# Kernel tuning notes

Hardware: AMD Instinct MI355X
Metric: run time of the kernel (lower is better)

The kernel has to match this reference:

```python
import jax, jax.numpy as jnp
import numpy as np


def _token2map(tok, loc, h, w):
    # scatter-add tokens onto an h x w grid. forward uses kernel_size=1, so the
    # Gaussian inpainting branch (reconstruct_feature) is a no-op and omitted.
    B, Nt, C = tok.shape
    loc = jnp.clip(loc, -1.0, 1.0)
    px = 0.5 * (loc + 1.0) * jnp.array([w, h], dtype=tok.dtype) - 0.5
    px = jnp.round(px).astype(jnp.int32)
    x0 = jnp.clip(px[..., 0], 0, w - 1)
    y0 = jnp.clip(px[..., 1], 0, h - 1)
    idx = (x0 + y0 * w + jnp.arange(B, dtype=jnp.int32)[:, None] * (h * w)).reshape(-1)
    src = jnp.concatenate([tok, jnp.ones((B, Nt, 1), tok.dtype)], axis=-1).reshape(B * Nt, C + 1)
    out = jnp.zeros((B * h * w, C + 1), tok.dtype).at[idx].add(src)
    out = out.reshape(B, h, w, C + 1)
    feat, mask = out[..., :C], out[..., C:]
    feat = feat / (mask + 1e-6)
    mask = (mask > 0).astype(tok.dtype)
    return feat * mask  # [B,h,w,C]


def setup_inputs():
    key = jax.random.key(0)
    ks = jax.random.split(key, 8)
    B, N, Nsrc, C = 8, 2048, 2048, 512
    H = W = 64
    return dict(
        x=jax.random.normal(ks[0], (B, N, C), jnp.float32),
        x_source=jax.random.normal(ks[1], (B, Nsrc, C), jnp.float32),
        loc_source=jax.random.normal(ks[2], (B, Nsrc, 2), jnp.float32),
        conf_source=jax.random.normal(ks[3], (B, Nsrc, 1), jnp.float32) * 0.1,
        q_w=jax.random.normal(ks[4], (C, C), jnp.float32) * 0.02,
        kv_w=jax.random.normal(ks[5], (2 * C, C), jnp.float32) * 0.02,
        sr_w=jax.random.normal(ks[6], (C, C), jnp.float32) * (2.0 / C) ** 0.5,
        sr_b=jnp.zeros((C,), jnp.float32),
        ln_g=jnp.ones((C,), jnp.float32),
        ln_b=jnp.zeros((C,), jnp.float32),
        proj_w=jax.random.normal(ks[7], (C, C), jnp.float32) * 0.02,
        proj_b=jnp.zeros((C,), jnp.float32),
        H=H, W=W,
    )


def reference(x, x_source, loc_source, conf_source, q_w, kv_w, sr_w, sr_b, ln_g, ln_b, proj_w, proj_b, H, W):
    num_heads, sr_ratio = 8, 2
    B, N, C = x.shape
    hd = C // num_heads
    scale = hd ** -0.5
    h, w = H // sr_ratio, W // sr_ratio
    # queries: [B, heads, N, hd]
    q = (x @ q_w.T).reshape(B, N, num_heads, hd).transpose(0, 2, 1, 3)
    # rasterize source tokens to a dense grid, then 1x1 conv (sr)
    feat = _token2map(x_source, loc_source, h, w)          # [B,h,w,C]
    xs = jnp.einsum('bhwi,oi->bhwo', feat, sr_w) + sr_b    # 1x1 conv == per-pixel linear
    xs = xs.reshape(B, h * w, C)                           # matches reshape(B,C,hw).permute(0,2,1)
    # LayerNorm (eps=1e-5) + exact GELU
    mu = xs.mean(-1, keepdims=True)
    var = ((xs - mu) ** 2).mean(-1, keepdims=True)
    xs = (xs - mu) / jnp.sqrt(var + 1e-5) * ln_g + ln_b
    xs = jax.nn.gelu(xs, approximate=False)
    # confidence rasterized the same way, added as attention bias
    conf = _token2map(conf_source, loc_source, h, w).reshape(B, h * w)  # [B,Ns]
    kv = (xs @ kv_w.T).reshape(B, h * w, 2, num_heads, hd).transpose(2, 0, 3, 1, 4)
    k, v = kv[0], kv[1]                                    # [B,heads,Ns,hd]
    attn = jnp.einsum('bhnd,bhmd->bhnm', q, k) * scale + conf[:, None, None, :]
    attn = jax.nn.softmax(attn, axis=-1)
    out = jnp.einsum('bhnm,bhmd->bhnd', attn, v).transpose(0, 2, 1, 3).reshape(B, N, C)
    return out @ proj_w.T + proj_b
```

## Files before the change

### kernel.cpp

```cpp
#include <hip/hip_runtime.h>
#include <math.h>

typedef unsigned short u16;
typedef __attribute__((ext_vector_type(8))) short short8;
typedef __attribute__((ext_vector_type(4))) float f32x4;
typedef __attribute__((ext_vector_type(4))) int   i32x4;

#define BB     8
#define NN     2048
#define CC     512
#define HEADS  8
#define HD     64
#define GM     1024

#define B_FEATF   ((size_t)0)
#define B_XSF     ((size_t)16*1024*1024)
#define B_XBF     ((size_t)32*1024*1024)
#define B_KB      ((size_t)48*1024*1024)
#define B_VT      ((size_t)56*1024*1024)
#define B_FEATBF  ((size_t)64*1024*1024)
#define B_XSBF    ((size_t)72*1024*1024)
#define B_CNT     ((size_t)80*1024*1024)
#define B_CONF    (B_CNT + (size_t)32*1024)
#define B_WQ      (B_CNT + (size_t)64*1024)
#define B_WKV     (B_WQ  + (size_t)512*1024)
#define B_WSR     (B_WKV + (size_t)1024*1024)
#define B_WPROJ   (B_WSR + (size_t)512*1024)

__device__ __forceinline__ u16 f2bf(float f) {
    unsigned u = __float_as_uint(f);
    unsigned r = (u + 0x7fffu + ((u >> 16) & 1u)) >> 16;
    return (u16)r;
}

__device__ __forceinline__ unsigned cvt_pk_bf16(float lo, float hi) {
    unsigned r;
    asm("v_cvt_pk_bf16_f32 %0, %1, %2" : "=v"(r) : "v"(lo), "v"(hi));
    return r;
}

__global__ __launch_bounds__(256) void cast_all_kernel(
    const float* __restrict__ x,      u16* __restrict__ x_bf,
    const float* __restrict__ q_w,    u16* __restrict__ wq_bf,
    const float* __restrict__ kv_w,   u16* __restrict__ wkv_bf,
    const float* __restrict__ sr_w,   u16* __restrict__ wsr_bf,
    const float* __restrict__ proj_w, u16* __restrict__ wpr_bf)
{
    const int bid = blockIdx.x;
    const float* src; u16* dst; int base;
    if      (bid < 8192) { src = x;      dst = x_bf;   base = bid; }
    else if (bid < 8448) { src = q_w;    dst = wq_bf;  base = bid - 8192; }
    else if (bid < 8960) { src = kv_w;   dst = wkv_bf; base = bid - 8448; }
    else if (bid < 9216) { src = sr_w;   dst = wsr_bf; base = bid - 8960; }
    else                 { src = proj_w; dst = wpr_bf; base = bid - 9216; }
    const int i = base * 256 + threadIdx.x;
    const float4 v = ((const float4*)src)[i];
    ushort4 o;
    o.x = f2bf(v.x); o.y = f2bf(v.y); o.z = f2bf(v.z); o.w = f2bf(v.w);
    ((ushort4*)dst)[i] = o;
}

__global__ __launch_bounds__(256) void scatter_idx_kernel(const float* __restrict__ loc,
    int* __restrict__ cnt_i, int* __restrict__ slots)
{
    const int token = blockIdx.x * 256 + threadIdx.x;
    const int b = token >> 11;
    float lx = loc[token * 2 + 0];
    float ly = loc[token * 2 + 1];
    lx = fminf(fmaxf(lx, -1.0f), 1.0f);
    ly = fminf(fmaxf(ly, -1.0f), 1.0f);
    const float pxf = rintf(0.5f * (lx + 1.0f) * 32.0f - 0.5f);
    const float pyf = rintf(0.5f * (ly + 1.0f) * 32.0f - 0.5f);
    int x0 = (int)pxf; x0 = min(max(x0, 0), 31);
    int y0 = (int)pyf; y0 = min(max(y0, 0), 31);
    const int row = b * GM + y0 * 32 + x0;
    const int slot = atomicAdd(&cnt_i[row], 1);
    if (slot < 128) slots[row * 128 + slot] = token;
}

__global__ __launch_bounds__(256) void gather_reduce_kernel(
    const float* __restrict__ x_source, const float* __restrict__ conf_src,
    const int* __restrict__ cnt_i, const int* __restrict__ slots,
    u16* __restrict__ featb, float* __restrict__ conf)
{
    const int row = blockIdx.x;
    const int tid = threadIdx.x;
    const int n0 = cnt_i[row];
    const int n = min(n0, 128);

    float a0 = 0.0f, a1 = 0.0f;
    #pragma unroll 2
    for (int t = 0; t < n; ++t) {
        const int tok = slots[row * 128 + t];
        const float* s = x_source + (size_t)tok * CC;
        a0 += s[tid];
        a1 += s[tid + 256];
    }

    __shared__ float cred[2];
    float cv = (tid < n) ? conf_src[slots[row * 128 + tid]] : 0.0f;
    if (tid < 128) {
        #pragma unroll
        for (int o = 32; o > 0; o >>= 1) cv += __shfl_down(cv, o, 64);
        if ((tid & 63) == 0) cred[tid >> 6] = cv;
    }
    __syncthreads();

    const float fn = (float)n0;
    const float sc = (n0 > 0) ? (1.0f / (fn + 1e-6f)) : 0.0f;
    u16* o = featb + (size_t)row * CC;
    o[tid]       = f2bf(a0 * sc);
    o[tid + 256] = f2bf(a1 * sc);
    if (tid == 0) conf[row] = (cred[0] + cred[1]) * sc;
}

template<bool BIAS, int OUTMODE>
__device__ __forceinline__ void gemm_body(int bx, int by,
    const u16* __restrict__ A, const u16* __restrict__ Bw,
    const float* __restrict__ bias,
    float* __restrict__ Cf, u16* __restrict__ Cb, u16* __restrict__ Vt,
    int M, int Nn, int K, u16* sm)
{
    u16* As = sm;
    u16* Bs = sm + 8192;
    const int tid = threadIdx.x;
    const int l = tid & 63, r = l & 15, g = l >> 4;
    const int w = tid >> 6, wm = w >> 1, wn = w & 1;
    const int m0 = by * 128, n0 = bx * 128;

    f32x4 acc[4][4] = {};
    const int nkt = K >> 5;

    #pragma unroll
    for (int it = 0; it < 2; ++it) {
        const int c = it * 256 + tid;
        const int row = c >> 2;
        const int gg = (c & 3) ^ ((row >> 2) & 3);
        __builtin_amdgcn_global_load_lds(A  + (size_t)(m0 + row) * K + gg * 8,
            (u16*)((char*)As + it * 4096 + (tid & 192) * 16), 16, 0, 0);
        __builtin_amdgcn_global_load_lds(Bw + (size_t)(n0 + row) * K + gg * 8,
            (u16*)((char*)Bs + it * 4096 + (tid & 192) * 16), 16, 0, 0);
    }
    __syncthreads();

    for (int kt = 0; kt < nkt; ++kt) {
        const int cur = kt & 1;
        if (kt + 1 < nkt) {
            #pragma unroll
            for (int it = 0; it < 2; ++it) {
                const int c = it * 256 + tid;
                const int row = c >> 2;
                const int gg = (c & 3) ^ ((row >> 2) & 3);
                __builtin_amdgcn_global_load_lds(A  + (size_t)(m0 + row) * K + (kt + 1) * 32 + gg * 8,
                    (u16*)((char*)As + (cur ^ 1) * 8192 + it * 4096 + (tid & 192) * 16), 16, 0, 0);
                __builtin_amdgcn_global_load_lds(Bw + (size_t)(n0 + row) * K + (kt + 1) * 32 + gg * 8,
                    (u16*)((char*)Bs + (cur ^ 1) * 8192 + it * 4096 + (tid & 192) * 16), 16, 0, 0);
            }
        }

        short8 af[4], bf[4];
        #pragma unroll
        for (int mi = 0; mi < 4; ++mi) {
            const int row = wm * 64 + mi * 16 + r;
            af[mi] = *(const short8*)((char*)As + cur * 8192 + row * 64 + ((g ^ (r >> 2)) & 3) * 16);
        }
        #pragma unroll
        for (int ni = 0; ni < 4; ++ni) {
            const int row = wn * 64 + ni * 16 + r;
            bf[ni] = *(const short8*)((char*)Bs + cur * 8192 + row * 64 + ((g ^ (r >> 2)) & 3) * 16);
        }
        #pragma unroll
        for (int mi = 0; mi < 4; ++mi)
            #pragma unroll
            for (int ni = 0; ni < 4; ++ni)
                acc[mi][ni] = __builtin_amdgcn_mfma_f32_16x16x32_bf16(af[mi], bf[ni], acc[mi][ni], 0, 0, 0);

        __syncthreads();
    }

    #pragma unroll
    for (int mi = 0; mi < 4; ++mi) {
        const int rbase = m0 + wm * 64 + mi * 16 + g * 4;
        #pragma unroll
        for (int ni = 0; ni < 4; ++ni) {
            const int col = n0 + wn * 64 + ni * 16 + r;
            const float bv = BIAS ? bias[col] : 0.0f;
            #pragma unroll
            for (int reg = 0; reg < 4; ++reg) {
                const float v = acc[mi][ni][reg] + bv;
                if (OUTMODE == 0) {
                    Cf[(size_t)(rbase + reg) * Nn + col] = v;
                } else if (OUTMODE == 1) {
                    Cb[(size_t)(rbase + reg) * Nn + col] = f2bf(v);
                } else if (OUTMODE == 3) {
                    Cb[(size_t)(rbase + reg) * Nn + col] = f2bf(v * 0.125f);
                } else {
                    const int f = rbase + reg;
                    const int head = f >> 6, d = f & 63;
                    const int bb2 = col >> 10, tok = col & 1023;
                    const int u = tok & 63;
                    const int S = ((u >> 5) << 5) | (((u >> 2) & 3) << 3)
                                | (((u >> 4) & 1) << 2) | (u & 3);
                    const int stok = (tok & ~63) | S;
                    Vt[(((size_t)bb2 * 8 + head) * 64 + d) * 1024 + stok] = f2bf(v);
                }
            }
        }
    }
}

template<bool BIAS, int OUTMODE>
__global__ __launch_bounds__(256) void gemm_single(const u16* __restrict__ A,
    const u16* __restrict__ Bw, const float* __restrict__ bias,
    float* __restrict__ Cf, u16* __restrict__ Cb, u16* __restrict__ Vt,
    int M, int Nn, int K)
{
    __shared__ u16 sm[16384];
    gemm_body<BIAS, OUTMODE>(blockIdx.x, blockIdx.y, A, Bw, bias, Cf, Cb, Vt, M, Nn, K, sm);
}

__global__ __launch_bounds__(256) void gemm_kvq_kernel(
    const u16* __restrict__ xs_bf, const u16* __restrict__ wkv_bf,
    u16* __restrict__ kb_bf, u16* __restrict__ vt_bf,
    const u16* __restrict__ x_bf, const u16* __restrict__ wq_bf,
    u16* __restrict__ q_bf)
{
    __shared__ u16 sm[16384];
    const int bid = blockIdx.x;
    if (bid < 256) {
        gemm_body<false, 1>(bid & 3, bid >> 2, xs_bf, wkv_bf, nullptr,
                            nullptr, kb_bf, nullptr, 8192, 512, 512, sm);
    } else if (bid < 512) {
        const int id = bid - 256;
        gemm_body<false, 2>(id & 63, id >> 6, wkv_bf + (size_t)512 * 512, xs_bf, nullptr,
                            nullptr, nullptr, vt_bf, 512, 8192, 512, sm);
    } else {
        const int id = bid - 512;
        gemm_body<false, 3>(id & 3, id >> 2, x_bf, wq_bf, nullptr,
                            nullptr, q_bf, nullptr, 16384, 512, 512, sm);
    }
}

__global__ __launch_bounds__(256) void ln_gelu_kernel(const float* __restrict__ xs,
    u16* __restrict__ xsb, const float* __restrict__ g, const float* __restrict__ bta)
{
    const int row = blockIdx.x;
    const int tid = threadIdx.x;
    const float2 v = *(const float2*)&xs[(size_t)row * CC + tid * 2];
    float s  = v.x + v.y;
    float ss = v.x * v.x + v.y * v.y;
    #pragma unroll
    for (int o = 32; o > 0; o >>= 1) { s += __shfl_down(s, o); ss += __shfl_down(ss, o); }
    __shared__ float red[10];
    const int wid = tid >> 6;
    if ((tid & 63) == 0) { red[wid] = s; red[4 + wid] = ss; }
    __syncthreads();
    if (tid == 0) {
        const float S  = red[0] + red[1] + red[2] + red[3];
        const float SS = red[4] + red[5] + red[6] + red[7];
        const float mu = S * (1.0f / 512.0f);
        const float var = SS * (1.0f / 512.0f) - mu * mu;
        red[8] = mu;
        red[9] = 1.0f / sqrtf(var + 1e-5f);
    }
    __syncthreads();
    const float mu = red[8], inv = red[9];
    const float2 gg = *(const float2*)&g[tid * 2];
    const float2 bb = *(const float2*)&bta[tid * 2];
    float x0 = (v.x - mu) * inv * gg.x + bb.x;
    float x1 = (v.y - mu) * inv * gg.y + bb.y;
    x0 = 0.5f * x0 * (1.0f + erff(x0 * 0.70710678118654752f));
    x1 = 0.5f * x1 * (1.0f + erff(x1 * 0.70710678118654752f));
    ushort2 o; o.x = f2bf(x0); o.y = f2bf(x1);
    *(ushort2*)&xsb[(size_t)row * CC + tid * 2] = o;
}

__global__ __launch_bounds__(256) void attn_mfma(const u16* __restrict__ q,
    const u16* __restrict__ kb, const u16* __restrict__ vt,
    const float* __restrict__ conf, u16* __restrict__ out)
{
    const int bid = blockIdx.x;
    const int xcd = bid & 7, slot = bid >> 3;
    const int bh = xcd * 8 + (slot & 7);
    const int qt = slot >> 3;
    const int b = bh >> 3, h = bh & 7;
    const int tid = threadIdx.x;
    const int l = tid & 63, r = l & 15, g = l >> 4;
    const int w = tid >> 6;

    __shared__ u16 Kl[8192];
    __shared__ float confs[1024];

    #pragma unroll
    for (int cc = 0; cc < 4; ++cc)
        confs[tid + cc * 256] = conf[b * GM + cc * 256 + tid];

    short8 qa[2], qb_[2];
    {
        const u16* qp = q + ((size_t)(b * NN + qt * 128 + w * 32 + r)) * CC + h * HD + g * 8;
        qa[0]  = *(const short8*)(qp);
        qa[1]  = *(const short8*)(qp + 32);
        qb_[0] = *(const short8*)(qp + 16 * CC);
        qb_[1] = *(const short8*)(qp + 16 * CC + 32);
    }

    const u16* vbase = vt + ((size_t)(b * 8 + h) * 64) * 1024;

    f32x4 oa[4] = {}, ob[4] = {};
    float ma = -1e30f, la = 0.0f, mb = -1e30f, lb = 0.0f;

    #pragma unroll
    for (int it = 0; it < 2; ++it) {
        const int c = it * 256 + tid;
        const int row = c >> 3, s = c & 7;
        const int gg = s ^ (row & 7);
        __builtin_amdgcn_global_load_lds(kb + ((size_t)(b * GM + row)) * 512 + h * HD + gg * 8,
            (u16*)((char*)Kl + it * 4096 + (tid & 192) * 16), 16, 0, 0);
    }
    __syncthreads();

    for (int kt = 0; kt < 16; ++kt) {
        const int cur = kt & 1;

        if (kt + 1 < 16) {
            #pragma unroll
            for (int it = 0; it < 2; ++it) {
                const int c = it * 256 + tid;
                const int row = c >> 3, s = c & 7;
                const int gg = s ^ (row & 7);
                __builtin_amdgcn_global_load_lds(
                    kb + ((size_t)(b * GM + (kt + 1) * 64 + row)) * 512 + h * HD + gg * 8,
                    (u16*)((char*)Kl + (cur ^ 1) * 8192 + it * 4096 + (tid & 192) * 16), 16, 0, 0);
            }
        }

        short8 vfr[2][4];
        #pragma unroll
        for (int ks = 0; ks < 2; ++ks)
            #pragma unroll
            for (int ni = 0; ni < 4; ++ni)
                vfr[ks][ni] = *(const short8*)(vbase + (size_t)(ni * 16 + r) * 1024
                                               + kt * 64 + ks * 32 + g * 8);

        f32x4 sa[4] = {}, sb[4] = {};
        #pragma unroll
        for (int ks = 0; ks < 2; ++ks)
            #pragma unroll
            for (int jt = 0; jt < 4; ++jt) {
                const int key = jt * 16 + r;
                const short8 kf = *(const short8*)((char*)Kl + cur * 8192 + key * 128 +
                                                   (((ks * 4 + g) ^ (key & 7)) * 16));
                sa[jt] = __builtin_amdgcn_mfma_f32_16x16x32_bf16(kf, qa[ks],  sa[jt], 0, 0, 0);
                sb[jt] = __builtin_amdgcn_mfma_f32_16x16x32_bf16(kf, qb_[ks], sb[jt], 0, 0, 0);
            }

        float tma = -1e30f, tmb = -1e30f;
        #pragma unroll
        for (int jt = 0; jt < 4; ++jt) {
            const f32x4 cf = *(const f32x4*)&confs[kt * 64 + jt * 16 + g * 4];
            #pragma unroll
            for (int reg = 0; reg < 4; ++reg) {
                sa[jt][reg] += cf[reg];
                sb[jt][reg] += cf[reg];
                tma = fmaxf(tma, sa[jt][reg]);
                tmb = fmaxf(tmb, sb[jt][reg]);
            }
        }
        tma = fmaxf(tma, __shfl_xor(tma, 16, 64));
        tma = fmaxf(tma, __shfl_xor(tma, 32, 64));
        tmb = fmaxf(tmb, __shfl_xor(tmb, 16, 64));
        tmb = fmaxf(tmb, __shfl_xor(tmb, 32, 64));

        if (!__all(tma <= ma + 8.0f)) {
            const float mta = fmaxf(ma, tma);
            const float rfa = __expf(ma - mta);
            ma = mta;
            la *= rfa;
            float rfq[4];
            #pragma unroll
            for (int reg = 0; reg < 4; ++reg) rfq[reg] = __shfl(rfa, g * 4 + reg, 64);
            #pragma unroll
            for (int ni = 0; ni < 4; ++ni)
                #pragma unroll
                for (int reg = 0; reg < 4; ++reg) oa[ni][reg] *= rfq[reg];
        }
        if (!__all(tmb <= mb + 8.0f)) {
            const float mtb = fmaxf(mb, tmb);
            const float rfb = __expf(mb - mtb);
            mb = mtb;
            lb *= rfb;
            float rfq[4];
            #pragma unroll
            for (int reg = 0; reg < 4; ++reg) rfq[reg] = __shfl(rfb, g * 4 + reg, 64);
            #pragma unroll
            for (int ni = 0; ni < 4; ++ni)
                #pragma unroll
                for (int reg = 0; reg < 4; ++reg) ob[ni][reg] *= rfq[reg];
        }

        float psa = 0.0f, psb = 0.0f;
        #pragma unroll
        for (int jt = 0; jt < 4; ++jt)
            #pragma unroll
            for (int reg = 0; reg < 4; ++reg) {
                const float eva = __expf(sa[jt][reg] - ma);
                const float evb = __expf(sb[jt][reg] - mb);
                sa[jt][reg] = eva; sb[jt][reg] = evb;
                psa += eva; psb += evb;
            }
        psa += __shfl_xor(psa, 16, 64);
        psa += __shfl_xor(psa, 32, 64);
        psb += __shfl_xor(psb, 16, 64);
        psb += __shfl_xor(psb, 32, 64);
        la += psa;
        lb += psb;

        unsigned wa[4][2], wb[4][2];
        #pragma unroll
        for (int jt = 0; jt < 4; ++jt) {
            wa[jt][0] = cvt_pk_bf16(sa[jt][0], sa[jt][1]);
            wa[jt][1] = cvt_pk_bf16(sa[jt][2], sa[jt][3]);
            wb[jt][0] = cvt_pk_bf16(sb[jt][0], sb[jt][1]);
            wb[jt][1] = cvt_pk_bf16(sb[jt][2], sb[jt][3]);
        }

        #pragma unroll
        for (int ks = 0; ks < 2; ++ks) {
            i32x4 pwa, pwb;
            pwa.x = (int)wa[2 * ks][0];     pwa.y = (int)wa[2 * ks][1];
            pwa.z = (int)wa[2 * ks + 1][0]; pwa.w = (int)wa[2 * ks + 1][1];
            pwb.x = (int)wb[2 * ks][0];     pwb.y = (int)wb[2 * ks][1];
            pwb.z = (int)wb[2 * ks + 1][0]; pwb.w = (int)wb[2 * ks + 1][1];
            const short8 paa = __builtin_bit_cast(short8, pwa);
            const short8 pab = __builtin_bit_cast(short8, pwb);
            #pragma unroll
            for (int ni = 0; ni < 4; ++ni) {
                oa[ni] = __builtin_amdgcn_mfma_f32_16x16x32_bf16(paa, vfr[ks][ni], oa[ni], 0, 0, 0);
                ob[ni] = __builtin_amdgcn_mfma_f32_16x16x32_bf16(pab, vfr[ks][ni], ob[ni], 0, 0, 0);
            }
        }

        __syncthreads();
    }

    float lqa[4], lqb[4];
    #pragma unroll
    for (int reg = 0; reg < 4; ++reg) {
        lqa[reg] = __shfl(la, g * 4 + reg, 64);
        lqb[reg] = __shfl(lb, g * 4 + reg, 64);
    }
    const size_t orowa = (size_t)(b * NN + qt * 128 + w * 32 + g * 4);
    #pragma unroll
    for (int ni = 0; ni < 4; ++ni)
        #pragma unroll
        for (int reg = 0; reg < 4; ++reg) {
            out[(orowa + reg) * CC + h * HD + ni * 16 + r]      = f2bf(oa[ni][reg] / lqa[reg]);
            out[(orowa + 16 + reg) * CC + h * HD + ni * 16 + r] = f2bf(ob[ni][reg] / lqb[reg]);
        }
}

extern "C" void kernel_launch(void* const* d_in, const int* in_sizes, int n_in,
                              void* d_out, int out_size, void* d_ws, size_t ws_size,
                              hipStream_t stream)
{
    (void)in_sizes; (void)n_in; (void)out_size; (void)ws_size;
    const float* x        = (const float*)d_in[0];
    const float* x_source = (const float*)d_in[1];
    const float* loc      = (const float*)d_in[2];
    const float* conf_src = (const float*)d_in[3];
    const float* q_w      = (const float*)d_in[4];
    const float* kv_w     = (const float*)d_in[5];
    const float* sr_w     = (const float*)d_in[6];
    const float* sr_b     = (const float*)d_in[7];
    const float* ln_g     = (const float*)d_in[8];
    const float* ln_b     = (const float*)d_in[9];
    const float* proj_w   = (const float*)d_in[10];
    const float* proj_b   = (const float*)d_in[11];

    char* ws = (char*)d_ws;
    int*   slots   = (int*)(ws + B_FEATF);
    float* xs      = (float*)(ws + B_XSF);
    int*   cnt_i   = (int*)(ws + B_CNT);
    float* conf    = (float*)(ws + B_CONF);
    u16*   x_bf    = (u16*)(ws + B_XBF);
    u16*   kb_bf   = (u16*)(ws + B_KB);
    u16*   vt_bf   = (u16*)(ws + B_VT);
    u16*   feat_bf = (u16*)(ws + B_FEATBF);
    u16*   xs_bf   = (u16*)(ws + B_XSBF);
    u16*   wq_bf   = (u16*)(ws + B_WQ);
    u16*   wkv_bf  = (u16*)(ws + B_WKV);
    u16*   wsr_bf  = (u16*)(ws + B_WSR);
    u16*   wpr_bf  = (u16*)(ws + B_WPROJ);
    u16*   q_bf    = (u16*)(ws + B_XSF);
    u16*   attn_bf = (u16*)(ws + B_FEATF);
    float* outp    = (float*)d_out;

    hipMemsetAsync(cnt_i, 0, 8192 * sizeof(int), stream);

    cast_all_kernel<<<9472, 256, 0, stream>>>(x, x_bf, q_w, wq_bf, kv_w, wkv_bf,
                                              sr_w, wsr_bf, proj_w, wpr_bf);

    scatter_idx_kernel<<<64, 256, 0, stream>>>(loc, cnt_i, slots);
    gather_reduce_kernel<<<8192, 256, 0, stream>>>(x_source, conf_src, cnt_i, slots,
                                                   feat_bf, conf);

    gemm_single<true, 0><<<dim3(4, 64), 256, 0, stream>>>(feat_bf, wsr_bf, sr_b,
                                                          xs, nullptr, nullptr, 8192, 512, 512);
    ln_gelu_kernel<<<8192, 256, 0, stream>>>(xs, xs_bf, ln_g, ln_b);

    gemm_kvq_kernel<<<1024, 256, 0, stream>>>(xs_bf, wkv_bf, kb_bf, vt_bf,
                                              x_bf, wq_bf, q_bf);

    attn_mfma<<<1024, 256, 0, stream>>>(q_bf, kb_bf, vt_bf, conf, attn_bf);

    gemm_single<true, 0><<<dim3(4, 128), 256, 0, stream>>>(attn_bf, wpr_bf, proj_b,
                                                           outp, nullptr, nullptr, 16384, 512, 512);
}
```

Baseline: 324.9 us.

## Store K in MFMA-fragment order and read it directly, drop LDS staging

The K projection epilogue now writes K in a per-(batch,head) layout that matches the MFMA operand fragment order. The attention kernel loads K fragments straight from global memory instead of double-buffering them through LDS, and reads conf from global instead of shared memory. This removes the LDS staging and the per-tile barrier. Softmax is moved to base-2 exponentials by folding log2(e) into the Q scale and conf, and the conditional lazy rescale is replaced by an unconditional one. The trade is more global and L2 traffic per wave and extra rescale multiplies on every tile, in exchange for fewer barriers and lower LDS use, which may allow more waves per CU.

```diff
diff --git a/kernel.cpp b/kernel.cpp
--- a/kernel.cpp
+++ b/kernel.cpp
@@ -12,6 +12,9 @@
 #define HEADS  8
 #define HD     64
 #define GM     1024
+
+#define LOG2E     1.44269504088896340736f
+#define QSCALE    (0.125f * LOG2E)
 
 #define B_FEATF   ((size_t)0)
 #define B_XSF     ((size_t)16*1024*1024)
@@ -111,7 +114,7 @@
     u16* o = featb + (size_t)row * CC;
     o[tid]       = f2bf(a0 * sc);
     o[tid + 256] = f2bf(a1 * sc);
-    if (tid == 0) conf[row] = (cred[0] + cred[1]) * sc;
+    if (tid == 0) conf[row] = (cred[0] + cred[1]) * sc * LOG2E;
 }
 
 template<bool BIAS, int OUTMODE>
@@ -190,11 +193,9 @@
                 const float v = acc[mi][ni][reg] + bv;
                 if (OUTMODE == 0) {
                     Cf[(size_t)(rbase + reg) * Nn + col] = v;
-                } else if (OUTMODE == 1) {
-                    Cb[(size_t)(rbase + reg) * Nn + col] = f2bf(v);
                 } else if (OUTMODE == 3) {
-                    Cb[(size_t)(rbase + reg) * Nn + col] = f2bf(v * 0.125f);
-                } else {
+                    Cb[(size_t)(rbase + reg) * Nn + col] = f2bf(v * QSCALE);
+                } else if (OUTMODE == 2) {
                     const int f = rbase + reg;
                     const int head = f >> 6, d = f & 63;
                     const int bb2 = col >> 10, tok = col & 1023;
@@ -203,6 +204,16 @@
                                 | (((u >> 4) & 1) << 2) | (u & 3);
                     const int stok = (tok & ~63) | S;
                     Vt[(((size_t)bb2 * 8 + head) * 64 + d) * 1024 + stok] = f2bf(v);
+                } else {
+                    const int f = col;
+                    const int hh = f >> 6, d = f & 63;
+                    const int kks = d >> 5, gg = (d >> 3) & 3, e = d & 7;
+                    const int t = rbase + reg;
+                    const int bb2 = t >> 10, tok = t & 1023;
+                    const int ktt = tok >> 6, key = tok & 63;
+                    const int jtt = key >> 4, rr = key & 15;
+                    Vt[(((((size_t)(bb2 * 8 + hh) * 16 + ktt) * 2 + kks) * 4 + jtt) * 64
+                        + (gg * 16 + rr)) * 8 + e] = f2bf(v);
                 }
             }
         }
@@ -221,15 +232,15 @@
 
 __global__ __launch_bounds__(256) void gemm_kvq_kernel(
     const u16* __restrict__ xs_bf, const u16* __restrict__ wkv_bf,
-    u16* __restrict__ kb_bf, u16* __restrict__ vt_bf,
+    u16* __restrict__ kf_bf, u16* __restrict__ vt_bf,
     const u16* __restrict__ x_bf, const u16* __restrict__ wq_bf,
     u16* __restrict__ q_bf)
 {
     __shared__ u16 sm[16384];
     const int bid = blockIdx.x;
     if (bid < 256) {
-        gemm_body<false, 1>(bid & 3, bid >> 2, xs_bf, wkv_bf, nullptr,
-                            nullptr, kb_bf, nullptr, 8192, 512, 512, sm);
+        gemm_body<false, 4>(bid & 3, bid >> 2, xs_bf, wkv_bf, nullptr,
+                            nullptr, nullptr, kf_bf, 8192, 512, 512, sm);
     } else if (bid < 512) {
         const int id = bid - 256;
         gemm_body<false, 2>(id & 63, id >> 6, wkv_bf + (size_t)512 * 512, xs_bf, nullptr,
@@ -276,7 +287,7 @@
 }
 
 __global__ __launch_bounds__(256) void attn_mfma(const u16* __restrict__ q,
-    const u16* __restrict__ kb, const u16* __restrict__ vt,
+    const u16* __restrict__ kf, const u16* __restrict__ vt,
     const float* __restrict__ conf, u16* __restrict__ out)
 {
     const int bid = blockIdx.x;
@@ -288,13 +299,6 @@
     const int l = tid & 63, r = l & 15, g = l >> 4;
     const int w = tid >> 6;
 
-    __shared__ u16 Kl[8192];
-    __shared__ float confs[1024];
-
-    #pragma unroll
-    for (int cc = 0; cc < 4; ++cc)
-        confs[tid + cc * 256] = conf[b * GM + cc * 256 + tid];
-
     short8 qa[2], qb_[2];
     {
         const u16* qp = q + ((size_t)(b * NN + qt * 128 + w * 32 + r)) * CC + h * HD + g * 8;
@@ -304,60 +308,33 @@
         qb_[1] = *(const short8*)(qp + 16 * CC + 32);
     }
 
-    const u16* vbase = vt + ((size_t)(b * 8 + h) * 64) * 1024;
+    const u16* kfb   = kf + (size_t)(b * 8 + h) * 65536;
+    const u16* vbase = vt + (size_t)(b * 8 + h) * 65536;
+    const float* confp = conf + b * GM;
 
     f32x4 oa[4] = {}, ob[4] = {};
     float ma = -1e30f, la = 0.0f, mb = -1e30f, lb = 0.0f;
 
-    #pragma unroll
-    for (int it = 0; it < 2; ++it) {
-        const int c = it * 256 + tid;
-        const int row = c >> 3, s = c & 7;
-        const int gg = s ^ (row & 7);
-        __builtin_amdgcn_global_load_lds(kb + ((size_t)(b * GM + row)) * 512 + h * HD + gg * 8,
-            (u16*)((char*)Kl + it * 4096 + (tid & 192) * 16), 16, 0, 0);
-    }
-    __syncthreads();
-
+    #pragma unroll 1
     for (int kt = 0; kt < 16; ++kt) {
-        const int cur = kt & 1;
-
-        if (kt + 1 < 16) {
-            #pragma unroll
-            for (int it = 0; it < 2; ++it) {
-                const int c = it * 256 + tid;
-                const int row = c >> 3, s = c & 7;
-                const int gg = s ^ (row & 7);
-                __builtin_amdgcn_global_load_lds(
-                    kb + ((size_t)(b * GM + (kt + 1) * 64 + row)) * 512 + h * HD + gg * 8,
-                    (u16*)((char*)Kl + (cur ^ 1) * 8192 + it * 4096 + (tid & 192) * 16), 16, 0, 0);
-            }
-        }
-
-        short8 vfr[2][4];
-        #pragma unroll
-        for (int ks = 0; ks < 2; ++ks)
-            #pragma unroll
-            for (int ni = 0; ni < 4; ++ni)
-                vfr[ks][ni] = *(const short8*)(vbase + (size_t)(ni * 16 + r) * 1024
-                                               + kt * 64 + ks * 32 + g * 8);
-
         f32x4 sa[4] = {}, sb[4] = {};
         #pragma unroll
-        for (int ks = 0; ks < 2; ++ks)
+        for (int ks = 0; ks < 2; ++ks) {
+            short8 kfr[4];
+            #pragma unroll
+            for (int jt = 0; jt < 4; ++jt)
+                kfr[jt] = *(const short8*)(kfb + (((kt * 2 + ks) * 4 + jt) << 9) + l * 8);
             #pragma unroll
             for (int jt = 0; jt < 4; ++jt) {
-                const int key = jt * 16 + r;
-                const short8 kf = *(const short8*)((char*)Kl + cur * 8192 + key * 128 +
-                                                   (((ks * 4 + g) ^ (key & 7)) * 16));
-                sa[jt] = __builtin_amdgcn_mfma_f32_16x16x32_bf16(kf, qa[ks],  sa[jt], 0, 0, 0);
-                sb[jt] = __builtin_amdgcn_mfma_f32_16x16x32_bf16(kf, qb_[ks], sb[jt], 0, 0, 0);
-            }
+                sa[jt] = __builtin_amdgcn_mfma_f32_16x16x32_bf16(kfr[jt], qa[ks],  sa[jt], 0, 0, 0);
+                sb[jt] = __builtin_amdgcn_mfma_f32_16x16x32_bf16(kfr[jt], qb_[ks], sb[jt], 0, 0, 0);
+            }
+        }
 
         float tma = -1e30f, tmb = -1e30f;
         #pragma unroll
         for (int jt = 0; jt < 4; ++jt) {
-            const f32x4 cf = *(const f32x4*)&confs[kt * 64 + jt * 16 + g * 4];
+            const f32x4 cf = *(const f32x4*)(confp + kt * 64 + jt * 16 + g * 4);
             #pragma unroll
             for (int reg = 0; reg < 4; ++reg) {
                 sa[jt][reg] += cf[reg];
@@ -371,40 +348,19 @@
         tmb = fmaxf(tmb, __shfl_xor(tmb, 16, 64));
         tmb = fmaxf(tmb, __shfl_xor(tmb, 32, 64));
 
-        if (!__all(tma <= ma + 8.0f)) {
-            const float mta = fmaxf(ma, tma);
-            const float rfa = __expf(ma - mta);
-            ma = mta;
-            la *= rfa;
-            float rfq[4];
-            #pragma unroll
-            for (int reg = 0; reg < 4; ++reg) rfq[reg] = __shfl(rfa, g * 4 + reg, 64);
-            #pragma unroll
-            for (int ni = 0; ni < 4; ++ni)
-                #pragma unroll
-                for (int reg = 0; reg < 4; ++reg) oa[ni][reg] *= rfq[reg];
-        }
-        if (!__all(tmb <= mb + 8.0f)) {
-            const float mtb = fmaxf(mb, tmb);
-            const float rfb = __expf(mb - mtb);
-            mb = mtb;
-            lb *= rfb;
-            float rfq[4];
-            #pragma unroll
-            for (int reg = 0; reg < 4; ++reg) rfq[reg] = __shfl(rfb, g * 4 + reg, 64);
-            #pragma unroll
-            for (int ni = 0; ni < 4; ++ni)
-                #pragma unroll
-                for (int reg = 0; reg < 4; ++reg) ob[ni][reg] *= rfq[reg];
-        }
+        const float mta = fmaxf(ma, tma);
+        const float mtb = fmaxf(mb, tmb);
+        const float rfa = __builtin_amdgcn_exp2f(ma - mta);
+        const float rfb = __builtin_amdgcn_exp2f(mb - mtb);
+        ma = mta; mb = mtb;
 
         float psa = 0.0f, psb = 0.0f;
         #pragma unroll
         for (int jt = 0; jt < 4; ++jt)
             #pragma unroll
             for (int reg = 0; reg < 4; ++reg) {
-                const float eva = __expf(sa[jt][reg] - ma);
-                const float evb = __expf(sb[jt][reg] - mb);
+                const float eva = __builtin_amdgcn_exp2f(sa[jt][reg] - ma);
+                const float evb = __builtin_amdgcn_exp2f(sb[jt][reg] - mb);
                 sa[jt][reg] = eva; sb[jt][reg] = evb;
                 psa += eva; psb += evb;
             }
@@ -412,8 +368,8 @@
         psa += __shfl_xor(psa, 32, 64);
         psb += __shfl_xor(psb, 16, 64);
         psb += __shfl_xor(psb, 32, 64);
-        la += psa;
-        lb += psb;
+        la = la * rfa + psa;
+        lb = lb * rfb + psb;
 
         unsigned wa[4][2], wb[4][2];
         #pragma unroll
@@ -424,8 +380,27 @@
             wb[jt][1] = cvt_pk_bf16(sb[jt][2], sb[jt][3]);
         }
 
+        float rfqa[4], rfqb[4];
+        #pragma unroll
+        for (int reg = 0; reg < 4; ++reg) {
+            rfqa[reg] = __shfl(rfa, g * 4 + reg, 64);
+            rfqb[reg] = __shfl(rfb, g * 4 + reg, 64);
+        }
+        #pragma unroll
+        for (int ni = 0; ni < 4; ++ni)
+            #pragma unroll
+            for (int reg = 0; reg < 4; ++reg) {
+                oa[ni][reg] *= rfqa[reg];
+                ob[ni][reg] *= rfqb[reg];
+            }
+
         #pragma unroll
         for (int ks = 0; ks < 2; ++ks) {
+            short8 vfr[4];
+            #pragma unroll
+            for (int ni = 0; ni < 4; ++ni)
+                vfr[ni] = *(const short8*)(vbase + (size_t)(ni * 16 + r) * 1024
+                                           + kt * 64 + ks * 32 + g * 8);
             i32x4 pwa, pwb;
             pwa.x = (int)wa[2 * ks][0];     pwa.y = (int)wa[2 * ks][1];
             pwa.z = (int)wa[2 * ks + 1][0]; pwa.w = (int)wa[2 * ks + 1][1];
@@ -435,12 +410,10 @@
             const short8 pab = __builtin_bit_cast(short8, pwb);
             #pragma unroll
             for (int ni = 0; ni < 4; ++ni) {
-                oa[ni] = __builtin_amdgcn_mfma_f32_16x16x32_bf16(paa, vfr[ks][ni], oa[ni], 0, 0, 0);
-                ob[ni] = __builtin_amdgcn_mfma_f32_16x16x32_bf16(pab, vfr[ks][ni], ob[ni], 0, 0, 0);
-            }
-        }
-
-        __syncthreads();
+                oa[ni] = __builtin_amdgcn_mfma_f32_16x16x32_bf16(paa, vfr[ni], oa[ni], 0, 0, 0);
+                ob[ni] = __builtin_amdgcn_mfma_f32_16x16x32_bf16(pab, vfr[ni], ob[ni], 0, 0, 0);
+            }
+        }
     }
 
     float lqa[4], lqb[4];
@@ -483,7 +456,7 @@
     int*   cnt_i   = (int*)(ws + B_CNT);
     float* conf    = (float*)(ws + B_CONF);
     u16*   x_bf    = (u16*)(ws + B_XBF);
-    u16*   kb_bf   = (u16*)(ws + B_KB);
+    u16*   kf_bf   = (u16*)(ws + B_KB);
     u16*   vt_bf   = (u16*)(ws + B_VT);
     u16*   feat_bf = (u16*)(ws + B_FEATBF);
     u16*   xs_bf   = (u16*)(ws + B_XSBF);
@@ -508,10 +481,10 @@
                                                           xs, nullptr, nullptr, 8192, 512, 512);
     ln_gelu_kernel<<<8192, 256, 0, stream>>>(xs, xs_bf, ln_g, ln_b);
 
-    gemm_kvq_kernel<<<1024, 256, 0, stream>>>(xs_bf, wkv_bf, kb_bf, vt_bf,
+    gemm_kvq_kernel<<<1024, 256, 0, stream>>>(xs_bf, wkv_bf, kf_bf, vt_bf,
                                               x_bf, wq_bf, q_bf);
 
-    attn_mfma<<<1024, 256, 0, stream>>>(q_bf, kb_bf, vt_bf, conf, attn_bf);
+    attn_mfma<<<1024, 256, 0, stream>>>(q_bf, kf_bf, vt_bf, conf, attn_bf);
 
     gemm_single<true, 0><<<dim3(4, 128), 256, 0, stream>>>(attn_bf, wpr_bf, proj_b,
                                                            outp, nullptr, nullptr, 16384, 512, 512);
```

Result: slower. 337.0 us (+3.7%).
